# Optimization experiments

Hardware: AMD Instinct MI355X
Metric: run time of the kernel (lower is better)

Reference implementation:

```python
import jax, jax.numpy as jnp
import numpy as np

N, H, W, C = 8, 64, 64, 256
G, KS = 4, 3
K = KS * KS                      # 9 kernel points (remove_center=False)
GD = C // G                      # 64 channels per group
OM_DIM = int(np.ceil(G * K * 3 / 8) * 8)   # 112 = offsets(72)+mask(36)+pad(4)
STRIDE = PAD = DIL = 1
OFFSET_SCALE = 1.0
SOFTMAX = False


def setup_inputs() -> dict:
    ks = jax.random.split(jax.random.key(0), 6)
    s = 0.02
    return {
        "x": jax.random.normal(ks[0], (N, H * W, C), jnp.float32),
        "shape_h": H,
        "shape_w": W,
        "w_in": jax.random.normal(ks[1], (C, C), jnp.float32) * s,
        "b_in": jnp.zeros((C,), jnp.float32),
        "w_out": jax.random.normal(ks[2], (C, C), jnp.float32) * s,
        "b_out": jnp.zeros((C,), jnp.float32),
        "w_dw": jax.random.normal(ks[3], (KS, KS, 1, C), jnp.float32) * s,  # depthwise HWIO
        "b_dw": jnp.zeros((C,), jnp.float32),
        "w_pw": jax.random.normal(ks[4], (OM_DIM, C), jnp.float32) * s,
        "b_pw": jnp.zeros((OM_DIM,), jnp.float32),
    }


def _deform_sample(xg, px, py, mask):
    # xg: [N, H*W, G, GD]; px/py/mask: [N, H, W, G, K]
    # Bilinear sample with zero padding outside the image, mask-weighted sum over K.
    n_idx = jnp.arange(N)[:, None, None, None, None]
    g_idx = jnp.arange(G)[None, None, None, :, None]
    x0 = jnp.floor(px)
    y0 = jnp.floor(py)
    out = jnp.zeros((N, H, W, G, GD), xg.dtype)
    for dy in (0, 1):
        for dx in (0, 1):
            xi = x0 + dx
            yi = y0 + dy
            wgt = (1.0 - jnp.abs(px - xi)) * (1.0 - jnp.abs(py - yi))
            valid = (xi >= 0) & (xi <= W - 1) & (yi >= 0) & (yi <= H - 1)
            wgt = jnp.where(valid, wgt, 0.0) * mask                     # [N,H,W,G,K]
            flat = (jnp.clip(yi, 0, H - 1) * W + jnp.clip(xi, 0, W - 1)).astype(jnp.int32)
            vals = xg[n_idx, flat, g_idx, :]                            # [N,H,W,G,K,GD]
            out = out + jnp.einsum("nhwgk,nhwgkc->nhwgc", wgt, vals)
    return out


def _forward(x, w_in, b_in, w_out, b_out, w_dw, b_dw, w_pw, b_pw):
    out = x @ w_in.T + b_in                                             # proj_input [N,L,C]
    # offset/mask branch runs on the raw (unprojected) input
    dw = jax.lax.conv_general_dilated(
        x.reshape(N, H, W, C), w_dw, (1, 1), [(PAD, PAD), (PAD, PAD)],
        dimension_numbers=("NHWC", "HWIO", "NHWC"), feature_group_count=C) + b_dw
    om = (dw.reshape(N, H * W, C) @ w_pw.T + b_pw).reshape(N, H, W, OM_DIM)
    off = om[..., : 2 * G * K].reshape(N, H, W, G, K, 2)                # (dx, dy)
    mask = om[..., 2 * G * K : 3 * G * K].reshape(N, H, W, G, K)
    if SOFTMAX:
        mask = jax.nn.softmax(mask, axis=-1)
    # sampling locations in input pixel coordinates (DCNv3 reference points)
    kk = (jnp.arange(KS) - (KS - 1) // 2) * DIL
    kgy, kgx = jnp.meshgrid(kk, kk, indexing="ij")
    kgx = kgx.reshape(-1).astype(x.dtype)                               # [K]
    kgy = kgy.reshape(-1).astype(x.dtype)
    base = (DIL * (KS - 1)) // 2 - PAD
    bx = (jnp.arange(W) * STRIDE + base).astype(x.dtype)
    by = (jnp.arange(H) * STRIDE + base).astype(x.dtype)
    px = bx[None, None, :, None, None] + OFFSET_SCALE * (kgx + off[..., 0])
    py = by[None, :, None, None, None] + OFFSET_SCALE * (kgy + off[..., 1])
    samp = _deform_sample(out.reshape(N, H * W, G, GD), px, py, mask)   # [N,H,W,G,GD]
    return samp.reshape(N, H * W, C) @ w_out.T + b_out                  # proj_output


def reference(x, shape_h, shape_w, w_in, b_in, w_out, b_out, w_dw, b_dw, w_pw, b_pw):
    assert (shape_h, shape_w) == (H, W)
    return _forward(x, w_in, b_in, w_out, b_out, w_dw, b_dw, w_pw, b_pw)
```

## Files before the change

kernel.cpp:

```cpp
#include <hip/hip_runtime.h>

#define HW     4096
#define M_ROWS 32768
#define OMD    112
#define OMP    128

typedef __attribute__((ext_vector_type(8))) short short8;
typedef __attribute__((ext_vector_type(4))) float f32x4;

__device__ inline unsigned short f2bf(float f) {
  union { float f; unsigned int u; } v; v.f = f;
  unsigned int u = v.u;
  u += 0x7fffu + ((u >> 16) & 1u);
  return (unsigned short)(u >> 16);
}
__device__ inline float bf2f(unsigned short h) {
  union { unsigned int u; float f; } v; v.u = ((unsigned int)h) << 16;
  return v.f;
}

__global__ __launch_bounds__(256) void prep_fused(
    const float* __restrict__ x, const float* __restrict__ w_dw,
    const float* __restrict__ b_dw, const float* __restrict__ w_in,
    const float* __restrict__ w_out, const float* __restrict__ w_pw,
    const float* __restrict__ b_pw, unsigned short* __restrict__ xb,
    unsigned short* __restrict__ dwb, unsigned short* __restrict__ wi_b,
    unsigned short* __restrict__ wo_b, unsigned short* __restrict__ wp_b,
    float* __restrict__ bpw_pad) {
  int bid = blockIdx.x;
  int tid = threadIdx.x;
  if (bid < 8192) {
    int idx = bid * 256 + tid;
    int c4 = (idx & 63) * 4;
    int pp = idx >> 6;
    int n = pp >> 12;
    int hw = pp & 4095;
    int h = hw >> 6, w = hw & 63;
    float4 bb = *(const float4*)&b_dw[c4];
    float a0 = bb.x, a1 = bb.y, a2 = bb.z, a3 = bb.w;
#pragma unroll
    for (int ky = 0; ky < 3; ++ky) {
      int iy = h + ky - 1;
      if (iy < 0 || iy > 63) continue;
#pragma unroll
      for (int kx = 0; kx < 3; ++kx) {
        int ix = w + kx - 1;
        if (ix < 0 || ix > 63) continue;
        float4 xv = *(const float4*)&x[((size_t)(n << 12) + iy * 64 + ix) * 256 + c4];
        float4 wv = *(const float4*)&w_dw[(ky * 3 + kx) * 256 + c4];
        a0 += xv.x * wv.x;
        a1 += xv.y * wv.y;
        a2 += xv.z * wv.z;
        a3 += xv.w * wv.w;
      }
    }
    ushort4 o;
    o.x = f2bf(a0); o.y = f2bf(a1); o.z = f2bf(a2); o.w = f2bf(a3);
    *(ushort4*)&dwb[(size_t)pp * 256 + c4] = o;
    float4 cv = *(const float4*)&x[(size_t)pp * 256 + c4];
    ushort4 oc;
    oc.x = f2bf(cv.x); oc.y = f2bf(cv.y); oc.z = f2bf(cv.z); oc.w = f2bf(cv.w);
    *(ushort4*)&xb[(size_t)pp * 256 + c4] = oc;
  } else {
    int idx = (bid - 8192) * 256 + tid;
    if (idx < 65536) {
      wi_b[idx] = f2bf(w_in[idx]);
    } else if (idx < 131072) {
      int i = idx - 65536;
      wo_b[i] = f2bf(w_out[i]);
    } else if (idx < 131072 + OMP * 256) {
      int i = idx - 131072;
      int o = i >> 8;
      wp_b[i] = (o < OMD) ? f2bf(w_pw[i]) : (unsigned short)0;
    } else if (idx < 131072 + OMP * 256 + OMP) {
      int i = idx - (131072 + OMP * 256);
      bpw_pad[i] = (i < OMD) ? b_pw[i] : 0.f;
    }
  }
}

__global__ __launch_bounds__(256) void gemm_mid(
    const unsigned short* __restrict__ dwb, const unsigned short* __restrict__ wp_b,
    const float* __restrict__ bpw, unsigned short* __restrict__ om,
    const unsigned short* __restrict__ xb, const unsigned short* __restrict__ wi_b,
    const float* __restrict__ b_in, unsigned short* __restrict__ vproj) {
  __shared__ __align__(16) unsigned short As[128 * 32];
  __shared__ __align__(16) unsigned short Bs[128 * 32];
  int tid = threadIdx.x;
  int wave = tid >> 6, lane = tid & 63;
  int wr = wave >> 1, wc = wave & 1;

  const unsigned short *A, *W;
  const float* bias;
  unsigned short* Cout;
  int NN, colB;
  size_t rowB;
  int bid = blockIdx.x;
  if (bid < 256) {
    int swz = (bid & 7) * 32 + (bid >> 3);
    A = dwb; W = wp_b; bias = bpw; Cout = om; NN = 128;
    rowB = (size_t)swz * 128; colB = 0;
  } else {
    int b = bid - 256;
    int swz = (b & 7) * 64 + (b >> 3);
    A = xb; W = wi_b; bias = b_in; Cout = vproj; NN = 256;
    rowB = (size_t)(swz >> 1) * 128; colB = (swz & 1) * 128;
  }

  f32x4 acc[4][4];
#pragma unroll
  for (int m = 0; m < 4; ++m)
#pragma unroll
    for (int n = 0; n < 4; ++n) acc[m][n] = (f32x4)(0.f);

  int arow = lane >> 2;
  int acol = (lane & 3) * 8;

  for (int k0 = 0; k0 < 256; k0 += 32) {
#pragma unroll
    for (int jj = 0; jj < 2; ++jj) {
      int j = wave * 2 + jj;
      const unsigned short* ga = A + (rowB + 16 * j + arow) * 256 + k0 + acol;
      __builtin_amdgcn_global_load_lds(
          (const __attribute__((address_space(1))) unsigned int*)ga,
          (__attribute__((address_space(3))) unsigned int*)(As + j * 512),
          16, 0, 0);
      const unsigned short* gb =
          W + ((size_t)(colB + 16 * j + arow)) * 256 + k0 + acol;
      __builtin_amdgcn_global_load_lds(
          (const __attribute__((address_space(1))) unsigned int*)gb,
          (__attribute__((address_space(3))) unsigned int*)(Bs + j * 512),
          16, 0, 0);
    }
    __syncthreads();

    short8 aF[4], bF[4];
#pragma unroll
    for (int m = 0; m < 4; ++m)
      aF[m] = *(const short8*)&As[(wr * 64 + m * 16 + (lane & 15)) * 32 +
                                  (lane >> 4) * 8];
#pragma unroll
    for (int n = 0; n < 4; ++n)
      bF[n] = *(const short8*)&Bs[(wc * 64 + n * 16 + (lane & 15)) * 32 +
                                  (lane >> 4) * 8];
#pragma unroll
    for (int m = 0; m < 4; ++m)
#pragma unroll
      for (int n = 0; n < 4; ++n)
        acc[m][n] = __builtin_amdgcn_mfma_f32_16x16x32_bf16(
            aF[m], bF[n], acc[m][n], 0, 0, 0);
    __syncthreads();
  }

#pragma unroll
  for (int n = 0; n < 4; ++n) {
    int col = colB + wc * 64 + n * 16 + (lane & 15);
    float bv = bias[col];
#pragma unroll
    for (int m = 0; m < 4; ++m) {
#pragma unroll
      for (int j = 0; j < 4; ++j) {
        size_t row = rowB + wr * 64 + m * 16 + (lane >> 4) * 4 + j;
        Cout[row * NN + col] = f2bf(acc[m][n][j] + bv);
      }
    }
  }
}

__global__ __launch_bounds__(256) void deform_sample_v5(
    const unsigned short* __restrict__ vproj, const unsigned short* __restrict__ om,
    unsigned short* __restrict__ samp) {
  __shared__ __align__(16) unsigned short s_v[144 * 64];
  __shared__ __align__(16) float4 s_wgt[576];
  __shared__ __align__(16) int4   s_off[576];

  int bid = blockIdx.x;
  int swz = (bid & 7) * 256 + (bid >> 3);
  int n = swz >> 8;
  int rem = swz & 255;
  int tile = rem >> 2;
  int g = rem & 3;
  int ty0 = (tile >> 3) << 3, tx0 = (tile & 7) << 3;
  int wy0 = ty0 - 2, wx0 = tx0 - 2;

  int tid = threadIdx.x;
  int wave = tid >> 6, lane = tid & 63;

  const unsigned short* vimg = vproj + ((size_t)n << 12) * 256;

#pragma unroll
  for (int i = 0; i < 5; ++i) {
    int seg = i * 4 + wave;
    if (seg < 18) {
      int f = seg * 1024 + lane * 16;
      int cell = f >> 7;
      int inner = (f >> 1) & 63;
      int r = cell / 12, c = cell - r * 12;
      int gy = min(max(wy0 + r, 0), 63);
      int gx = min(max(wx0 + c, 0), 63);
      const unsigned short* src =
          vimg + (size_t)(gy * 64 + gx) * 256 + g * 64 + inner;
      __builtin_amdgcn_global_load_lds(
          (const __attribute__((address_space(1))) unsigned int*)src,
          (__attribute__((address_space(3))) unsigned int*)(s_v + seg * 512),
          16, 0, 0);
    }
  }

  for (int e = tid; e < 576; e += 256) {
    int pl = e / 9, k = e - pl * 9;
    int hy = ty0 + (pl >> 3), wx = tx0 + (pl & 7);
    int p = (n << 12) + hy * 64 + wx;
    int gk = g * 9 + k;
    const unsigned short* o = om + (size_t)p * OMP;
    float ox = bf2f(o[gk * 2]), oy = bf2f(o[gk * 2 + 1]);
    float msk = bf2f(o[72 + gk]);
    float px = (float)(wx + (k % 3) - 1) + ox;
    float py = (float)(hy + (k / 3) - 1) + oy;
    float x0f = floorf(px), y0f = floorf(py);
    int x0 = (int)x0f, y0 = (int)y0f;
    float fx = px - x0f, fy = py - y0f;
    bool vx0 = (unsigned)x0 < 64u, vx1 = (unsigned)(x0 + 1) < 64u;
    bool vy0 = (unsigned)y0 < 64u, vy1 = (unsigned)(y0 + 1) < 64u;
    float4 wv;
    wv.x = (vy0 && vx0) ? (1.f - fx) * (1.f - fy) * msk : 0.f;
    wv.y = (vy0 && vx1) ? fx * (1.f - fy) * msk : 0.f;
    wv.z = (vy1 && vx0) ? (1.f - fx) * fy * msk : 0.f;
    wv.w = (vy1 && vx1) ? fx * fy * msk : 0.f;
    int ix0 = min(max(min(max(x0, 0), 63) - wx0, 0), 11);
    int ix1 = min(max(min(max(x0 + 1, 0), 63) - wx0, 0), 11);
    int iy0 = min(max(min(max(y0, 0), 63) - wy0, 0), 11);
    int iy1 = min(max(min(max(y0 + 1, 0), 63) - wy0, 0), 11);
    int4 ov;
    ov.x = (iy0 * 12 + ix0) * 128;
    ov.y = (iy0 * 12 + ix1) * 128;
    ov.z = (iy1 * 12 + ix0) * 128;
    ov.w = (iy1 * 12 + ix1) * 128;
    s_wgt[e] = wv;
    s_off[e] = ov;
  }
  __syncthreads();

  int sub = lane & 7;
  int chb = sub * 16;
  const char* vb = (const char*)s_v;

#pragma unroll
  for (int iter = 0; iter < 2; ++iter) {
    int pl = iter * 32 + wave * 8 + (lane >> 3);
    int hy = ty0 + (pl >> 3), wx = tx0 + (pl & 7);
    int p = (n << 12) + hy * 64 + wx;

    float acc[8];
#pragma unroll
    for (int j = 0; j < 8; ++j) acc[j] = 0.f;

#pragma unroll
    for (int k = 0; k < 9; ++k) {
      int e = pl * 9 + k;
      float4 wv = s_wgt[e];
      int4 ov = s_off[e];
      short8 v00 = *(const short8*)(vb + ov.x + chb);
      short8 v01 = *(const short8*)(vb + ov.y + chb);
      short8 v10 = *(const short8*)(vb + ov.z + chb);
      short8 v11 = *(const short8*)(vb + ov.w + chb);
#pragma unroll
      for (int j = 0; j < 8; ++j)
        acc[j] += wv.x * bf2f((unsigned short)v00[j]) +
                  wv.y * bf2f((unsigned short)v01[j]) +
                  wv.z * bf2f((unsigned short)v10[j]) +
                  wv.w * bf2f((unsigned short)v11[j]);
    }

    union { unsigned short s[8]; short8 v8; } o8;
#pragma unroll
    for (int j = 0; j < 8; ++j) o8.s[j] = f2bf(acc[j]);
    *(short8*)&samp[(size_t)p * 256 + g * 64 + sub * 8] = o8.v8;
  }
}

__global__ __launch_bounds__(256) void gemm_out(
    const unsigned short* __restrict__ A, const unsigned short* __restrict__ W,
    const float* __restrict__ bias, float* __restrict__ Cout) {
  __shared__ __align__(16) unsigned short As[128 * 32];
  __shared__ __align__(16) unsigned short Bs[128 * 32];
  int tid = threadIdx.x;
  int wave = tid >> 6, lane = tid & 63;
  int wr = wave >> 1, wc = wave & 1;

  int bid = blockIdx.x;
  int swz = (bid & 7) * 64 + (bid >> 3);
  size_t rowB = (size_t)(swz >> 1) * 128;
  int colB = (swz & 1) * 128;

  f32x4 acc[4][4];
#pragma unroll
  for (int m = 0; m < 4; ++m)
#pragma unroll
    for (int n = 0; n < 4; ++n) acc[m][n] = (f32x4)(0.f);

  int arow = lane >> 2;
  int acol = (lane & 3) * 8;

  for (int k0 = 0; k0 < 256; k0 += 32) {
#pragma unroll
    for (int jj = 0; jj < 2; ++jj) {
      int j = wave * 2 + jj;
      const unsigned short* ga = A + (rowB + 16 * j + arow) * 256 + k0 + acol;
      __builtin_amdgcn_global_load_lds(
          (const __attribute__((address_space(1))) unsigned int*)ga,
          (__attribute__((address_space(3))) unsigned int*)(As + j * 512),
          16, 0, 0);
      const unsigned short* gb =
          W + ((size_t)(colB + 16 * j + arow)) * 256 + k0 + acol;
      __builtin_amdgcn_global_load_lds(
          (const __attribute__((address_space(1))) unsigned int*)gb,
          (__attribute__((address_space(3))) unsigned int*)(Bs + j * 512),
          16, 0, 0);
    }
    __syncthreads();

    short8 aF[4], bF[4];
#pragma unroll
    for (int m = 0; m < 4; ++m)
      aF[m] = *(const short8*)&As[(wr * 64 + m * 16 + (lane & 15)) * 32 +
                                  (lane >> 4) * 8];
#pragma unroll
    for (int n = 0; n < 4; ++n)
      bF[n] = *(const short8*)&Bs[(wc * 64 + n * 16 + (lane & 15)) * 32 +
                                  (lane >> 4) * 8];
#pragma unroll
    for (int m = 0; m < 4; ++m)
#pragma unroll
      for (int n = 0; n < 4; ++n)
        acc[m][n] = __builtin_amdgcn_mfma_f32_16x16x32_bf16(
            aF[m], bF[n], acc[m][n], 0, 0, 0);
    __syncthreads();
  }

#pragma unroll
  for (int n = 0; n < 4; ++n) {
    int col = colB + wc * 64 + n * 16 + (lane & 15);
    float bv = bias[col];
#pragma unroll
    for (int m = 0; m < 4; ++m) {
#pragma unroll
      for (int j = 0; j < 4; ++j) {
        size_t row = rowB + wr * 64 + m * 16 + (lane >> 4) * 4 + j;
        Cout[row * 256 + col] = acc[m][n][j] + bv;
      }
    }
  }
}

extern "C" void kernel_launch(void* const* d_in, const int* in_sizes, int n_in,
                              void* d_out, int out_size, void* d_ws,
                              size_t ws_size, hipStream_t stream) {
  const float* x     = (const float*)d_in[0];
  const float* w_in  = (const float*)d_in[3];
  const float* b_in  = (const float*)d_in[4];
  const float* w_out = (const float*)d_in[5];
  const float* b_out = (const float*)d_in[6];
  const float* w_dw  = (const float*)d_in[7];
  const float* b_dw  = (const float*)d_in[8];
  const float* w_pw  = (const float*)d_in[9];
  const float* b_pw  = (const float*)d_in[10];
  float* out = (float*)d_out;
  char* ws = (char*)d_ws;

  unsigned short* xb    = (unsigned short*)(ws);
  unsigned short* dwb   = (unsigned short*)(ws + (16u << 20));
  unsigned short* vproj = (unsigned short*)(ws + (32u << 20));
  unsigned short* om    = (unsigned short*)(ws + (48u << 20));
  unsigned short* wi_b  = (unsigned short*)(ws + (56u << 20));
  unsigned short* wo_b  = (unsigned short*)(ws + (56u << 20) + (128u << 10));
  unsigned short* wp_b  = (unsigned short*)(ws + (56u << 20) + (256u << 10));
  float*          bpw   = (float*)(ws + (56u << 20) + (320u << 10));

  prep_fused<<<8834, 256, 0, stream>>>(x, w_dw, b_dw, w_in, w_out, w_pw, b_pw,
                                       xb, dwb, wi_b, wo_b, wp_b, bpw);
  gemm_mid<<<768, 256, 0, stream>>>(dwb, wp_b, bpw, om, xb, wi_b, b_in, vproj);
  deform_sample_v5<<<2048, 256, 0, stream>>>(vproj, om, dwb );
  gemm_out<<<512, 256, 0, stream>>>(dwb, wo_b, b_out, out);
}
```

Baseline: 81.42 us.

## Double-buffer GEMM LDS staging and regroup offset/mask layout per group

Both GEMM kernels now use two LDS buffers, so the next K-slice is loaded asynchronously while the current one is multiplied, with explicit vmcnt waits and barriers. gemm_mid writes the offset/mask output in a per-group layout of 32 channels: 18 offsets, 9 masks and padding. This lets the deformable sampling kernel fetch each pixel's group parameters with a few vector loads from one thread per pixel instead of scattered scalar loads. The trade-offs are twice the LDS footprint and weight computation done by only 64 threads instead of 256.

```diff
diff --git a/kernel.cpp b/kernel.cpp
--- a/kernel.cpp
+++ b/kernel.cpp
@@ -6,6 +6,7 @@
 #define OMP    128
 
 typedef __attribute__((ext_vector_type(8))) short short8;
+typedef __attribute__((ext_vector_type(8), aligned(4))) short short8a;
 typedef __attribute__((ext_vector_type(4))) float f32x4;
 
 __device__ inline unsigned short f2bf(float f) {
@@ -84,8 +85,8 @@
     const float* __restrict__ bpw, unsigned short* __restrict__ om,
     const unsigned short* __restrict__ xb, const unsigned short* __restrict__ wi_b,
     const float* __restrict__ b_in, unsigned short* __restrict__ vproj) {
-  __shared__ __align__(16) unsigned short As[128 * 32];
-  __shared__ __align__(16) unsigned short Bs[128 * 32];
+  __shared__ __align__(16) unsigned short As[2][128 * 32];
+  __shared__ __align__(16) unsigned short Bs[2][128 * 32];
   int tid = threadIdx.x;
   int wave = tid >> 6, lane = tid & 63;
   int wr = wave >> 1, wc = wave & 1;
@@ -96,7 +97,8 @@
   int NN, colB;
   size_t rowB;
   int bid = blockIdx.x;
-  if (bid < 256) {
+  bool is_om = (bid < 256);
+  if (is_om) {
     int swz = (bid & 7) * 32 + (bid >> 3);
     A = dwb; W = wp_b; bias = bpw; Cout = om; NN = 128;
     rowB = (size_t)swz * 128; colB = 0;
@@ -116,58 +118,80 @@
   int arow = lane >> 2;
   int acol = (lane & 3) * 8;
 
-  for (int k0 = 0; k0 < 256; k0 += 32) {
+  auto STAGE = [&](int buf, int k0) {
 #pragma unroll
     for (int jj = 0; jj < 2; ++jj) {
       int j = wave * 2 + jj;
       const unsigned short* ga = A + (rowB + 16 * j + arow) * 256 + k0 + acol;
       __builtin_amdgcn_global_load_lds(
           (const __attribute__((address_space(1))) unsigned int*)ga,
-          (__attribute__((address_space(3))) unsigned int*)(As + j * 512),
+          (__attribute__((address_space(3))) unsigned int*)(As[buf] + j * 512),
           16, 0, 0);
       const unsigned short* gb =
           W + ((size_t)(colB + 16 * j + arow)) * 256 + k0 + acol;
       __builtin_amdgcn_global_load_lds(
           (const __attribute__((address_space(1))) unsigned int*)gb,
-          (__attribute__((address_space(3))) unsigned int*)(Bs + j * 512),
+          (__attribute__((address_space(3))) unsigned int*)(Bs[buf] + j * 512),
           16, 0, 0);
     }
-    __syncthreads();
+  };
+
+  STAGE(0, 0);
+  int cur = 0;
+  for (int t = 0; t < 8; ++t) {
+    if (t < 7) {
+      STAGE(cur ^ 1, (t + 1) * 32);
+      asm volatile("s_waitcnt vmcnt(4)" ::: "memory");
+    } else {
+      asm volatile("s_waitcnt vmcnt(0)" ::: "memory");
+    }
+    __builtin_amdgcn_sched_barrier(0);
+    __builtin_amdgcn_s_barrier();
 
     short8 aF[4], bF[4];
 #pragma unroll
     for (int m = 0; m < 4; ++m)
-      aF[m] = *(const short8*)&As[(wr * 64 + m * 16 + (lane & 15)) * 32 +
-                                  (lane >> 4) * 8];
+      aF[m] = *(const short8*)&As[cur][(wr * 64 + m * 16 + (lane & 15)) * 32 +
+                                       (lane >> 4) * 8];
 #pragma unroll
     for (int n = 0; n < 4; ++n)
-      bF[n] = *(const short8*)&Bs[(wc * 64 + n * 16 + (lane & 15)) * 32 +
-                                  (lane >> 4) * 8];
+      bF[n] = *(const short8*)&Bs[cur][(wc * 64 + n * 16 + (lane & 15)) * 32 +
+                                       (lane >> 4) * 8];
 #pragma unroll
     for (int m = 0; m < 4; ++m)
 #pragma unroll
       for (int n = 0; n < 4; ++n)
         acc[m][n] = __builtin_amdgcn_mfma_f32_16x16x32_bf16(
             aF[m], bF[n], acc[m][n], 0, 0, 0);
-    __syncthreads();
+
+    asm volatile("s_waitcnt lgkmcnt(0)" ::: "memory");
+    __builtin_amdgcn_sched_barrier(0);
+    __builtin_amdgcn_s_barrier();
+    cur ^= 1;
   }
 
 #pragma unroll
   for (int n = 0; n < 4; ++n) {
-    int col = colB + wc * 64 + n * 16 + (lane & 15);
-    float bv = bias[col];
+    int c = colB + wc * 64 + n * 16 + (lane & 15);
+    float bv = bias[c];
+    int nc = c;
+    if (is_om) {
+      if (c < 72)       nc = (c / 18) * 32 + (c % 18);
+      else if (c < 108) { int u = c - 72;  nc = (u / 9) * 32 + 18 + (u % 9); }
+      else              { int u = c - 108; nc = (u / 5) * 32 + 27 + (u % 5); }
+    }
 #pragma unroll
     for (int m = 0; m < 4; ++m) {
 #pragma unroll
       for (int j = 0; j < 4; ++j) {
         size_t row = rowB + wr * 64 + m * 16 + (lane >> 4) * 4 + j;
-        Cout[row * NN + col] = f2bf(acc[m][n][j] + bv);
+        Cout[row * NN + nc] = f2bf(acc[m][n][j] + bv);
       }
     }
   }
 }
 
-__global__ __launch_bounds__(256) void deform_sample_v5(
+__global__ __launch_bounds__(256) void deform_sample_v6(
     const unsigned short* __restrict__ vproj, const unsigned short* __restrict__ om,
     unsigned short* __restrict__ samp) {
   __shared__ __align__(16) unsigned short s_v[144 * 64];
@@ -207,37 +231,57 @@
     }
   }
 
-  for (int e = tid; e < 576; e += 256) {
-    int pl = e / 9, k = e - pl * 9;
+  if (tid < 64) {
+    int pl = tid;
     int hy = ty0 + (pl >> 3), wx = tx0 + (pl & 7);
     int p = (n << 12) + hy * 64 + wx;
-    int gk = g * 9 + k;
-    const unsigned short* o = om + (size_t)p * OMP;
-    float ox = bf2f(o[gk * 2]), oy = bf2f(o[gk * 2 + 1]);
-    float msk = bf2f(o[72 + gk]);
-    float px = (float)(wx + (k % 3) - 1) + ox;
-    float py = (float)(hy + (k / 3) - 1) + oy;
-    float x0f = floorf(px), y0f = floorf(py);
-    int x0 = (int)x0f, y0 = (int)y0f;
-    float fx = px - x0f, fy = py - y0f;
-    bool vx0 = (unsigned)x0 < 64u, vx1 = (unsigned)(x0 + 1) < 64u;
-    bool vy0 = (unsigned)y0 < 64u, vy1 = (unsigned)(y0 + 1) < 64u;
-    float4 wv;
-    wv.x = (vy0 && vx0) ? (1.f - fx) * (1.f - fy) * msk : 0.f;
-    wv.y = (vy0 && vx1) ? fx * (1.f - fy) * msk : 0.f;
-    wv.z = (vy1 && vx0) ? (1.f - fx) * fy * msk : 0.f;
-    wv.w = (vy1 && vx1) ? fx * fy * msk : 0.f;
-    int ix0 = min(max(min(max(x0, 0), 63) - wx0, 0), 11);
-    int ix1 = min(max(min(max(x0 + 1, 0), 63) - wx0, 0), 11);
-    int iy0 = min(max(min(max(y0, 0), 63) - wy0, 0), 11);
-    int iy1 = min(max(min(max(y0 + 1, 0), 63) - wy0, 0), 11);
-    int4 ov;
-    ov.x = (iy0 * 12 + ix0) * 128;
-    ov.y = (iy0 * 12 + ix1) * 128;
-    ov.z = (iy1 * 12 + ix0) * 128;
-    ov.w = (iy1 * 12 + ix1) * 128;
-    s_wgt[e] = wv;
-    s_off[e] = ov;
+    const unsigned short* o = om + (size_t)p * OMP + g * 32;
+    short8 xy0 = *(const short8*)(o);
+    short8 xy1 = *(const short8*)(o + 8);
+    unsigned int xy8 = *(const unsigned int*)(o + 16);
+    short8a mk = *(const short8a*)(o + 18);
+    unsigned short mk8 = o[26];
+
+#pragma unroll
+    for (int k = 0; k < 9; ++k) {
+      float ox, oy, msk;
+      if (k < 4) {
+        ox = bf2f((unsigned short)xy0[2 * k]);
+        oy = bf2f((unsigned short)xy0[2 * k + 1]);
+        msk = bf2f((unsigned short)mk[k]);
+      } else if (k < 8) {
+        ox = bf2f((unsigned short)xy1[2 * (k - 4)]);
+        oy = bf2f((unsigned short)xy1[2 * (k - 4) + 1]);
+        msk = bf2f((unsigned short)mk[k]);
+      } else {
+        ox = bf2f((unsigned short)(xy8 & 0xffffu));
+        oy = bf2f((unsigned short)(xy8 >> 16));
+        msk = bf2f(mk8);
+      }
+      float px = (float)(wx + (k % 3) - 1) + ox;
+      float py = (float)(hy + (k / 3) - 1) + oy;
+      float x0f = floorf(px), y0f = floorf(py);
+      int x0 = (int)x0f, y0 = (int)y0f;
+      float fx = px - x0f, fy = py - y0f;
+      bool vx0 = (unsigned)x0 < 64u, vx1 = (unsigned)(x0 + 1) < 64u;
+      bool vy0 = (unsigned)y0 < 64u, vy1 = (unsigned)(y0 + 1) < 64u;
+      float4 wv;
+      wv.x = (vy0 && vx0) ? (1.f - fx) * (1.f - fy) * msk : 0.f;
+      wv.y = (vy0 && vx1) ? fx * (1.f - fy) * msk : 0.f;
+      wv.z = (vy1 && vx0) ? (1.f - fx) * fy * msk : 0.f;
+      wv.w = (vy1 && vx1) ? fx * fy * msk : 0.f;
+      int ix0 = min(max(min(max(x0, 0), 63) - wx0, 0), 11);
+      int ix1 = min(max(min(max(x0 + 1, 0), 63) - wx0, 0), 11);
+      int iy0 = min(max(min(max(y0, 0), 63) - wy0, 0), 11);
+      int iy1 = min(max(min(max(y0 + 1, 0), 63) - wy0, 0), 11);
+      int4 ov;
+      ov.x = (iy0 * 12 + ix0) * 128;
+      ov.y = (iy0 * 12 + ix1) * 128;
+      ov.z = (iy1 * 12 + ix0) * 128;
+      ov.w = (iy1 * 12 + ix1) * 128;
+      s_wgt[pl * 9 + k] = wv;
+      s_off[pl * 9 + k] = ov;
+    }
   }
   __syncthreads();
 
@@ -282,8 +326,8 @@
 __global__ __launch_bounds__(256) void gemm_out(
     const unsigned short* __restrict__ A, const unsigned short* __restrict__ W,
     const float* __restrict__ bias, float* __restrict__ Cout) {
-  __shared__ __align__(16) unsigned short As[128 * 32];
-  __shared__ __align__(16) unsigned short Bs[128 * 32];
+  __shared__ __align__(16) unsigned short As[2][128 * 32];
+  __shared__ __align__(16) unsigned short Bs[2][128 * 32];
   int tid = threadIdx.x;
   int wave = tid >> 6, lane = tid & 63;
   int wr = wave >> 1, wc = wave & 1;
@@ -302,40 +346,56 @@
   int arow = lane >> 2;
   int acol = (lane & 3) * 8;
 
-  for (int k0 = 0; k0 < 256; k0 += 32) {
+  auto STAGE = [&](int buf, int k0) {
 #pragma unroll
     for (int jj = 0; jj < 2; ++jj) {
       int j = wave * 2 + jj;
       const unsigned short* ga = A + (rowB + 16 * j + arow) * 256 + k0 + acol;
       __builtin_amdgcn_global_load_lds(
           (const __attribute__((address_space(1))) unsigned int*)ga,
-          (__attribute__((address_space(3))) unsigned int*)(As + j * 512),
+          (__attribute__((address_space(3))) unsigned int*)(As[buf] + j * 512),
           16, 0, 0);
       const unsigned short* gb =
           W + ((size_t)(colB + 16 * j + arow)) * 256 + k0 + acol;
       __builtin_amdgcn_global_load_lds(
           (const __attribute__((address_space(1))) unsigned int*)gb,
-          (__attribute__((address_space(3))) unsigned int*)(Bs + j * 512),
+          (__attribute__((address_space(3))) unsigned int*)(Bs[buf] + j * 512),
           16, 0, 0);
     }
-    __syncthreads();
+  };
+
+  STAGE(0, 0);
+  int cur = 0;
+  for (int t = 0; t < 8; ++t) {
+    if (t < 7) {
+      STAGE(cur ^ 1, (t + 1) * 32);
+      asm volatile("s_waitcnt vmcnt(4)" ::: "memory");
+    } else {
+      asm volatile("s_waitcnt vmcnt(0)" ::: "memory");
+    }
+    __builtin_amdgcn_sched_barrier(0);
+    __builtin_amdgcn_s_barrier();
 
     short8 aF[4], bF[4];
 #pragma unroll
     for (int m = 0; m < 4; ++m)
-      aF[m] = *(const short8*)&As[(wr * 64 + m * 16 + (lane & 15)) * 32 +
-                                  (lane >> 4) * 8];
+      aF[m] = *(const short8*)&As[cur][(wr * 64 + m * 16 + (lane & 15)) * 32 +
+                                       (lane >> 4) * 8];
 #pragma unroll
     for (int n = 0; n < 4; ++n)
-      bF[n] = *(const short8*)&Bs[(wc * 64 + n * 16 + (lane & 15)) * 32 +
-                                  (lane >> 4) * 8];
+      bF[n] = *(const short8*)&Bs[cur][(wc * 64 + n * 16 + (lane & 15)) * 32 +
+                                       (lane >> 4) * 8];
 #pragma unroll
     for (int m = 0; m < 4; ++m)
 #pragma unroll
       for (int n = 0; n < 4; ++n)
         acc[m][n] = __builtin_amdgcn_mfma_f32_16x16x32_bf16(
             aF[m], bF[n], acc[m][n], 0, 0, 0);
-    __syncthreads();
+
+    asm volatile("s_waitcnt lgkmcnt(0)" ::: "memory");
+    __builtin_amdgcn_sched_barrier(0);
+    __builtin_amdgcn_s_barrier();
+    cur ^= 1;
   }
 
 #pragma unroll
@@ -380,6 +440,6 @@
   prep_fused<<<8834, 256, 0, stream>>>(x, w_dw, b_dw, w_in, w_out, w_pw, b_pw,
                                        xb, dwb, wi_b, wo_b, wp_b, bpw);
   gemm_mid<<<768, 256, 0, stream>>>(dwb, wp_b, bpw, om, xb, wi_b, b_in, vproj);
-  deform_sample_v5<<<2048, 256, 0, stream>>>(vproj, om, dwb );
+  deform_sample_v6<<<2048, 256, 0, stream>>>(vproj, om, dwb );
   gemm_out<<<512, 256, 0, stream>>>(dwb, wo_b, b_out, out);
 }
```

Result: slower. 83.08 us (+2.0%).
